# Performance work log

Hardware: AMD Instinct MI355X
Metric: run time of the kernel (lower is better)

## Reference

```python
import jax, jax.numpy as jnp
import numpy as np

B, NU, NI, D, L = 8, 1024, 2048, 64, 2
NUM_USERS, NUM_ITEMS = 100000, 50000


def setup_inputs() -> dict:
    key = jax.random.key(0)
    ks = jax.random.split(key, 9)
    return {
        "user_indices": jax.random.randint(ks[0], (B, NU), 0, NUM_USERS),
        "item_indices": jax.random.randint(ks[1], (B, NI), 0, NUM_ITEMS),
        "adj_matrices": jax.random.uniform(ks[2], (B, NU + NI, NU + NI), dtype=jnp.float32),
        "user_table": jax.random.normal(ks[3], (NUM_USERS, D), dtype=jnp.float32),
        "item_table": jax.random.normal(ks[4], (NUM_ITEMS, D), dtype=jnp.float32),
        "gc_w": jax.random.normal(ks[5], (L, D, D), dtype=jnp.float32) * 0.05,
        "gc_b": jax.random.normal(ks[6], (L, D), dtype=jnp.float32) * 0.05,
        "bi_w": jax.random.normal(ks[7], (L, D, D), dtype=jnp.float32) * 0.05,
        "bi_b": jax.random.normal(ks[8], (L, D), dtype=jnp.float32) * 0.05,
    }


def reference(user_indices, item_indices, adj_matrices, user_table, item_table, gc_w, gc_b, bi_w, bi_b):
    n_layers = gc_w.shape[0]

    def per_sample(u_idx, i_idx, adj):
        u_emb = user_table[u_idx]            # [NU, D]
        i_emb = item_table[i_idx]            # [NI, D]
        ego = jnp.concatenate([u_emb, i_emb], axis=0)  # [N, D]
        all_embs = [ego]
        for l in range(n_layers):
            side = adj @ ego                                        # [N, D]
            s = jax.nn.leaky_relu(side @ gc_w[l].T + gc_b[l])       # Linear(out,in) -> x @ W.T + b
            bi = jax.nn.leaky_relu((ego * side) @ bi_w[l].T + bi_b[l])
            ego = s + bi
            all_embs.append(ego)
        all_e = jnp.concatenate(all_embs, axis=1)                   # [N, D*(L+1)]
        u_g, i_g = all_e[: u_emb.shape[0]], all_e[u_emb.shape[0]:]
        scores = u_g @ i_g.T                                        # [NU, NI]
        return jax.nn.log_softmax(scores, axis=1)

    return jax.vmap(per_sample)(user_indices, item_indices, adj_matrices)
```

## Files before the change

kernel.cpp:

```cpp
#include <hip/hip_runtime.h>
#include <cstddef>

#define BB   8
#define NUU  1024
#define NII  2048
#define NTOT 3072
#define DD   64
#define KCAT 192

typedef __attribute__((ext_vector_type(8))) short bf16x8;
typedef __attribute__((ext_vector_type(4))) float f32x4;

__device__ __forceinline__ unsigned short f2bf(float f) {
  unsigned u = __float_as_uint(f);
  return (unsigned short)((u + 0x7fffu + ((u >> 16) & 1u)) >> 16);
}
__device__ __forceinline__ float bf2f(unsigned short s) {
  return __uint_as_float(((unsigned)s) << 16);
}
__device__ __forceinline__ uint4 pack8(float4 a, float4 b) {
  uint4 r;
  r.x = (unsigned)f2bf(a.x) | ((unsigned)f2bf(a.y) << 16);
  r.y = (unsigned)f2bf(a.z) | ((unsigned)f2bf(a.w) << 16);
  r.z = (unsigned)f2bf(b.x) | ((unsigned)f2bf(b.y) << 16);
  r.w = (unsigned)f2bf(b.z) | ((unsigned)f2bf(b.w) << 16);
  return r;
}
__device__ __forceinline__ bf16x8 u4_to_bf(uint4 u) {
  union { uint4 a; bf16x8 b; } x; x.a = u; return x.b;
}

__global__ __launch_bounds__(256) void transpose_w(
    const float* __restrict__ gcw, const float* __restrict__ biw,
    float* __restrict__ wT) {
  int g = blockIdx.x * 256 + threadIdx.x;
  int m = g >> 12, r = g & 4095;
  int k = r >> 6, d = r & 63;
  const float* src = (m < 2) ? gcw + m * 4096 : biw + (m - 2) * 4096;
  wT[g] = src[d * 64 + k];
}

__global__ __launch_bounds__(256) void gather_bf16(
    const int* __restrict__ uidx, const int* __restrict__ iidx,
    const float* __restrict__ utab, const float* __restrict__ itab,
    unsigned short* __restrict__ ecat) {
  int g = blockIdx.x * 256 + threadIdx.x;
  int node_g = g >> 2;
  int f0 = (g & 3) * 16;
  int b = node_g / NTOT;
  int row = node_g - b * NTOT;
  const float* src = (row < NUU) ? utab + (size_t)uidx[b * NUU + row] * DD
                                 : itab + (size_t)iidx[b * NII + row - NUU] * DD;
  const float4* s4 = reinterpret_cast<const float4*>(src + f0);
  uint4 lo = pack8(s4[0], s4[1]);
  uint4 hi = pack8(s4[2], s4[3]);
  uint4* dst = reinterpret_cast<uint4*>(ecat + (size_t)node_g * KCAT + f0);
  dst[0] = lo; dst[1] = hi;
}

__global__ __launch_bounds__(256) void conv_t(
    const unsigned short* __restrict__ ecat, int c0,
    unsigned short* __restrict__ Et) {
  __shared__ unsigned short T[64][65];
  const int tid = threadIdx.x;
  const int b = blockIdx.y;
  const int r0 = blockIdx.x * 64;
  {
    int nl = tid >> 2, fg = (tid & 3) * 16;
    const uint4* src = reinterpret_cast<const uint4*>(
        ecat + ((size_t)b * NTOT + r0 + nl) * KCAT + c0 + fg);
    uint4 v0 = src[0], v1 = src[1];
    unsigned short tmp[16];
    *reinterpret_cast<uint4*>(tmp) = v0;
    *reinterpret_cast<uint4*>(tmp + 8) = v1;
#pragma unroll
    for (int j = 0; j < 16; j++) T[fg + j][nl] = tmp[j];
  }
  __syncthreads();
  {
    int f = tid >> 2, ng = (tid & 3) * 16;
    unsigned short tmp[16];
#pragma unroll
    for (int j = 0; j < 16; j++) tmp[j] = T[f][ng + j];
    uint4* dst = reinterpret_cast<uint4*>(
        Et + ((size_t)b * DD + f) * NTOT + r0 + ng);
    dst[0] = *reinterpret_cast<uint4*>(tmp);
    dst[1] = *reinterpret_cast<uint4*>(tmp + 8);
  }
}

template <int CONV>
__global__ __launch_bounds__(256) void side_mfma_t(
    const float* __restrict__ adj, unsigned short* __restrict__ adjb,
    const unsigned short* __restrict__ Et, float* __restrict__ sp) {
  __shared__ __align__(16) unsigned short Bs[2][64][68];
  const int tid = threadIdx.x;
  const int w = tid >> 6, l = tid & 63;
  const int lane15 = l & 15, quad = l >> 4;
  const int b = blockIdx.z, kz = blockIdx.y;
  const int m0 = blockIdx.x * 128 + w * 16;
  const int kbase = kz * 768;
  const size_t row0 = (size_t)b * NTOT * NTOT +
                      (size_t)(m0 + lane15) * NTOT + kbase + quad * 8;
  const size_t row1 = row0 + (size_t)64 * NTOT;
  const float* A32_0 = adj + row0;
  const float* A32_1 = adj + row1;
  const unsigned short* A16_0 = adjb + row0;
  const unsigned short* A16_1 = adjb + row1;
  unsigned short* Aw_0 = adjb + row0;
  unsigned short* Aw_1 = adjb + row1;

  const int sf = tid >> 3, ss = (tid & 7) * 8;
  const unsigned short* Eb = Et + (size_t)b * DD * NTOT + kbase;
  uint4 p0 = *reinterpret_cast<const uint4*>(Eb + (size_t)sf * NTOT + ss);
  uint4 p1 = *reinterpret_cast<const uint4*>(Eb + (size_t)(sf + 32) * NTOT + ss);

  bf16x8 a0_0, a1_0, a0_1, a1_1;
  float4 f0_0, f1_0, f2_0, f3_0, f0_1, f1_1, f2_1, f3_1;
  if (CONV) {
    f0_0 = *reinterpret_cast<const float4*>(A32_0 + 0);
    f1_0 = *reinterpret_cast<const float4*>(A32_0 + 4);
    f2_0 = *reinterpret_cast<const float4*>(A32_0 + 32);
    f3_0 = *reinterpret_cast<const float4*>(A32_0 + 36);
    f0_1 = *reinterpret_cast<const float4*>(A32_1 + 0);
    f1_1 = *reinterpret_cast<const float4*>(A32_1 + 4);
    f2_1 = *reinterpret_cast<const float4*>(A32_1 + 32);
    f3_1 = *reinterpret_cast<const float4*>(A32_1 + 36);
  } else {
    a0_0 = *reinterpret_cast<const bf16x8*>(A16_0);
    a1_0 = *reinterpret_cast<const bf16x8*>(A16_0 + 32);
    a0_1 = *reinterpret_cast<const bf16x8*>(A16_1);
    a1_1 = *reinterpret_cast<const bf16x8*>(A16_1 + 32);
  }

  f32x4 acc[2][4];
#pragma unroll
  for (int s = 0; s < 2; s++)
#pragma unroll
    for (int t = 0; t < 4; t++) acc[s][t] = (f32x4){0.f, 0.f, 0.f, 0.f};

  for (int c = 0; c < 12; c++) {
    const int buf = c & 1;
    __syncthreads();
    *reinterpret_cast<uint4*>(&Bs[buf][sf][ss]) = p0;
    *reinterpret_cast<uint4*>(&Bs[buf][sf + 32][ss]) = p1;
    __syncthreads();

    if (CONV) {
      uint4 u0 = pack8(f0_0, f1_0), u1 = pack8(f2_0, f3_0);
      *reinterpret_cast<uint4*>(Aw_0 + c * 64) = u0;
      *reinterpret_cast<uint4*>(Aw_0 + c * 64 + 32) = u1;
      a0_0 = u4_to_bf(u0);
      a1_0 = u4_to_bf(u1);
      uint4 u2 = pack8(f0_1, f1_1), u3 = pack8(f2_1, f3_1);
      *reinterpret_cast<uint4*>(Aw_1 + c * 64) = u2;
      *reinterpret_cast<uint4*>(Aw_1 + c * 64 + 32) = u3;
      a0_1 = u4_to_bf(u2);
      a1_1 = u4_to_bf(u3);
    }

    bf16x8 na0_0, na1_0, na0_1, na1_1;
    if (c + 1 < 12) {
      p0 = *reinterpret_cast<const uint4*>(Eb + (size_t)sf * NTOT + (c + 1) * 64 + ss);
      p1 = *reinterpret_cast<const uint4*>(Eb + (size_t)(sf + 32) * NTOT + (c + 1) * 64 + ss);
      if (CONV) {
        f0_0 = *reinterpret_cast<const float4*>(A32_0 + (c + 1) * 64);
        f1_0 = *reinterpret_cast<const float4*>(A32_0 + (c + 1) * 64 + 4);
        f2_0 = *reinterpret_cast<const float4*>(A32_0 + (c + 1) * 64 + 32);
        f3_0 = *reinterpret_cast<const float4*>(A32_0 + (c + 1) * 64 + 36);
        f0_1 = *reinterpret_cast<const float4*>(A32_1 + (c + 1) * 64);
        f1_1 = *reinterpret_cast<const float4*>(A32_1 + (c + 1) * 64 + 4);
        f2_1 = *reinterpret_cast<const float4*>(A32_1 + (c + 1) * 64 + 32);
        f3_1 = *reinterpret_cast<const float4*>(A32_1 + (c + 1) * 64 + 36);
      } else {
        na0_0 = *reinterpret_cast<const bf16x8*>(A16_0 + (c + 1) * 64);
        na1_0 = *reinterpret_cast<const bf16x8*>(A16_0 + (c + 1) * 64 + 32);
        na0_1 = *reinterpret_cast<const bf16x8*>(A16_1 + (c + 1) * 64);
        na1_1 = *reinterpret_cast<const bf16x8*>(A16_1 + (c + 1) * 64 + 32);
      }
    }

#pragma unroll
    for (int t = 0; t < 4; t++) {
      bf16x8 b0 = *reinterpret_cast<const bf16x8*>(&Bs[buf][t * 16 + lane15][quad * 8]);
      acc[0][t] = __builtin_amdgcn_mfma_f32_16x16x32_bf16(a0_0, b0, acc[0][t], 0, 0, 0);
      acc[1][t] = __builtin_amdgcn_mfma_f32_16x16x32_bf16(a0_1, b0, acc[1][t], 0, 0, 0);
    }
#pragma unroll
    for (int t = 0; t < 4; t++) {
      bf16x8 b1 = *reinterpret_cast<const bf16x8*>(&Bs[buf][t * 16 + lane15][32 + quad * 8]);
      acc[0][t] = __builtin_amdgcn_mfma_f32_16x16x32_bf16(a1_0, b1, acc[0][t], 0, 0, 0);
      acc[1][t] = __builtin_amdgcn_mfma_f32_16x16x32_bf16(a1_1, b1, acc[1][t], 0, 0, 0);
    }
    if (!CONV && (c + 1 < 12)) {
      a0_0 = na0_0; a1_0 = na1_0; a0_1 = na0_1; a1_1 = na1_1;
    }
  }

  float* S = sp + ((size_t)kz * BB + b) * ((size_t)NTOT * DD);
#pragma unroll
  for (int s = 0; s < 2; s++)
#pragma unroll
    for (int t = 0; t < 4; t++)
#pragma unroll
      for (int r = 0; r < 4; r++)
        S[(size_t)(m0 + s * 64 + quad * 4 + r) * DD + t * 16 + lane15] =
            acc[s][t][r];
}

__global__ __launch_bounds__(256) void layer_post(
    const float* __restrict__ sp, unsigned short* __restrict__ ecat, int cin,
    const float* __restrict__ wTg, const float* __restrict__ wTb,
    const float* __restrict__ gcb, const float* __restrict__ bib) {
  __shared__ float wG[4096];
  __shared__ float wB[4096];
  __shared__ float rowS[4][64];
  __shared__ float rowE[4][64];
  const int tid = threadIdx.x;
#pragma unroll
  for (int i = 0; i < 16; i++) {
    int idx = tid + i * 256;
    wG[idx] = wTg[idx];
    wB[idx] = wTb[idx];
  }
  const int wv = tid >> 6, lane = tid & 63;
  const size_t row = (size_t)blockIdx.x * 4 + wv;
  const size_t off = row * DD + lane;
  const size_t P = (size_t)BB * NTOT * DD;
  float sv = sp[off] + sp[P + off] + sp[2 * P + off] + sp[3 * P + off];
  float ev = bf2f(ecat[row * KCAT + cin + lane]);
  rowS[wv][lane] = sv;
  rowE[wv][lane] = ev;
  __syncthreads();
  float sacc = gcb[lane];
  float bacc = bib[lane];
#pragma unroll 8
  for (int k = 0; k < 64; k++) {
    float sk = rowS[wv][k];
    float ek = rowE[wv][k];
    sacc += sk * wG[k * 64 + lane];
    bacc += (ek * sk) * wB[k * 64 + lane];
  }
  float s  = sacc > 0.f ? sacc : 0.01f * sacc;
  float bi = bacc > 0.f ? bacc : 0.01f * bacc;
  ecat[row * KCAT + cin + 64 + lane] = f2bf(s + bi);
}

__global__ __launch_bounds__(256) void scores_mfma(
    const unsigned short* __restrict__ ecat, float* __restrict__ out) {
  __shared__ __align__(16) unsigned short Ut[64 * KCAT];
  __shared__ __align__(16) unsigned short It[64 * KCAT];
  const int tid = threadIdx.x;
  const int w = tid >> 6, l = tid & 63;
  const int lane15 = l & 15, quad = l >> 4;
  const int b = blockIdx.z;
  const int u0 = blockIdx.y * 64;
  const int i0 = blockIdx.x * 64;
#pragma unroll
  for (int it = 0; it < 6; it++) {
    int idx = tid + it * 256;
    int row = idx / 24, c = idx - row * 24;
    int cs = c ^ (row & 7);
    uint4 vu = reinterpret_cast<const uint4*>(
        ecat + ((size_t)b * NTOT + u0 + row) * KCAT)[c];
    uint4 vi = reinterpret_cast<const uint4*>(
        ecat + ((size_t)b * NTOT + NUU + i0 + row) * KCAT)[c];
    reinterpret_cast<uint4*>(Ut)[row * 24 + cs] = vu;
    reinterpret_cast<uint4*>(It)[row * 24 + cs] = vi;
  }
  __syncthreads();
  f32x4 acc[4];
#pragma unroll
  for (int t = 0; t < 4; t++) acc[t] = (f32x4){0.f, 0.f, 0.f, 0.f};
  const int urow = w * 16 + lane15;
#pragma unroll
  for (int ks = 0; ks < 6; ks++) {
    int cu = (ks * 4 + quad) ^ (urow & 7);
    bf16x8 af = reinterpret_cast<const bf16x8*>(Ut)[urow * 24 + cu];
#pragma unroll
    for (int t = 0; t < 4; t++) {
      int irow = t * 16 + lane15;
      int ci = (ks * 4 + quad) ^ (irow & 7);
      bf16x8 bf = reinterpret_cast<const bf16x8*>(It)[irow * 24 + ci];
      acc[t] = __builtin_amdgcn_mfma_f32_16x16x32_bf16(af, bf, acc[t], 0, 0, 0);
    }
  }
  float* O = out + (size_t)b * NUU * NII;
#pragma unroll
  for (int t = 0; t < 4; t++)
#pragma unroll
    for (int r = 0; r < 4; r++)
      O[(size_t)(u0 + w * 16 + quad * 4 + r) * NII + i0 + t * 16 + lane15] =
          acc[t][r];
}

__global__ __launch_bounds__(256) void logsoftmax_kernel(float* __restrict__ out) {
  __shared__ float rm[4];
  __shared__ float rs[4];
  const int tid = threadIdx.x;
  const int lane = tid & 63, wv = tid >> 6;
  float* row = out + (size_t)blockIdx.x * NII;
  float4 v0 = *reinterpret_cast<const float4*>(row + tid * 4);
  float4 v1 = *reinterpret_cast<const float4*>(row + 1024 + tid * 4);
  float m = fmaxf(fmaxf(fmaxf(v0.x, v0.y), fmaxf(v0.z, v0.w)),
                  fmaxf(fmaxf(v1.x, v1.y), fmaxf(v1.z, v1.w)));
#pragma unroll
  for (int off = 32; off > 0; off >>= 1) m = fmaxf(m, __shfl_xor(m, off));
  if (lane == 0) rm[wv] = m;
  __syncthreads();
  m = fmaxf(fmaxf(rm[0], rm[1]), fmaxf(rm[2], rm[3]));
  float s = expf(v0.x - m) + expf(v0.y - m) + expf(v0.z - m) + expf(v0.w - m) +
            expf(v1.x - m) + expf(v1.y - m) + expf(v1.z - m) + expf(v1.w - m);
#pragma unroll
  for (int off = 32; off > 0; off >>= 1) s += __shfl_xor(s, off);
  if (lane == 0) rs[wv] = s;
  __syncthreads();
  float lse = m + logf(rs[0] + rs[1] + rs[2] + rs[3]);
  v0.x -= lse; v0.y -= lse; v0.z -= lse; v0.w -= lse;
  v1.x -= lse; v1.y -= lse; v1.z -= lse; v1.w -= lse;
  *reinterpret_cast<float4*>(row + tid * 4) = v0;
  *reinterpret_cast<float4*>(row + 1024 + tid * 4) = v1;
}

extern "C" void kernel_launch(void* const* d_in, const int* in_sizes, int n_in,
                              void* d_out, int out_size, void* d_ws, size_t ws_size,
                              hipStream_t stream) {
  (void)in_sizes; (void)n_in; (void)out_size; (void)ws_size;
  const int*   uidx = (const int*)d_in[0];
  const int*   iidx = (const int*)d_in[1];
  const float* adj  = (const float*)d_in[2];
  const float* utab = (const float*)d_in[3];
  const float* itab = (const float*)d_in[4];
  const float* gcw  = (const float*)d_in[5];
  const float* gcb  = (const float*)d_in[6];
  const float* biw  = (const float*)d_in[7];
  const float* bib  = (const float*)d_in[8];
  float* out = (float*)d_out;

  unsigned short* ecat = (unsigned short*)d_ws;
  unsigned short* Et   = ecat + (size_t)BB * NTOT * KCAT;
  unsigned short* adjb = Et + (size_t)BB * DD * NTOT;
  float* sp = (float*)d_out;
  const size_t P = (size_t)BB * NTOT * DD;
  float* wT = (float*)d_out + 4 * P;

  transpose_w<<<dim3(64), 256, 0, stream>>>(gcw, biw, wT);
  gather_bf16<<<dim3(BB * NTOT * 4 / 256), 256, 0, stream>>>(uidx, iidx, utab, itab, ecat);
  conv_t<<<dim3(48, BB), 256, 0, stream>>>(ecat, 0, Et);
  side_mfma_t<1><<<dim3(24, 4, BB), 256, 0, stream>>>(adj, adjb, Et, sp);
  layer_post<<<dim3(BB * NTOT / 4), 256, 0, stream>>>(sp, ecat, 0, wT, wT + 2 * 4096, gcb, bib);
  conv_t<<<dim3(48, BB), 256, 0, stream>>>(ecat, 64, Et);
  side_mfma_t<0><<<dim3(24, 4, BB), 256, 0, stream>>>(adj, adjb, Et, sp);
  layer_post<<<dim3(BB * NTOT / 4), 256, 0, stream>>>(sp, ecat, 64, wT + 4096, wT + 3 * 4096, gcb + 64, bib + 64);
  scores_mfma<<<dim3(32, 16, BB), 256, 0, stream>>>(ecat, out);
  logsoftmax_kernel<<<dim3(BB * NUU), 256, 0, stream>>>(out);
}
```

Before: 625.7 us.

## Fuse scores with log-softmax in LDS and fuse gather with transpose

Score computation and log-softmax are merged: each block computes 16 user rows against all items via MFMA, stages the scores in a large LDS buffer, and writes normalized output once, removing the extra read and rewrite of the big output. The gather, first-layer transpose and weight transpose are combined into one kernel to cut launches and a global round trip. The large LDS allocation limits occupancy to about one block per CU, and item embeddings are re-read by every block.

Result: slower. 651.8 us (+4.2%).

```diff
diff --git a/kernel.cpp b/kernel.cpp
--- a/kernel.cpp
+++ b/kernel.cpp
@@ -30,32 +30,52 @@
   union { uint4 a; bf16x8 b; } x; x.a = u; return x.b;
 }
 
-__global__ __launch_bounds__(256) void transpose_w(
-    const float* __restrict__ gcw, const float* __restrict__ biw,
-    float* __restrict__ wT) {
-  int g = blockIdx.x * 256 + threadIdx.x;
-  int m = g >> 12, r = g & 4095;
-  int k = r >> 6, d = r & 63;
-  const float* src = (m < 2) ? gcw + m * 4096 : biw + (m - 2) * 4096;
-  wT[g] = src[d * 64 + k];
-}
-
-__global__ __launch_bounds__(256) void gather_bf16(
+__global__ __launch_bounds__(256) void gather_t(
     const int* __restrict__ uidx, const int* __restrict__ iidx,
     const float* __restrict__ utab, const float* __restrict__ itab,
-    unsigned short* __restrict__ ecat) {
-  int g = blockIdx.x * 256 + threadIdx.x;
-  int node_g = g >> 2;
-  int f0 = (g & 3) * 16;
-  int b = node_g / NTOT;
-  int row = node_g - b * NTOT;
-  const float* src = (row < NUU) ? utab + (size_t)uidx[b * NUU + row] * DD
-                                 : itab + (size_t)iidx[b * NII + row - NUU] * DD;
-  const float4* s4 = reinterpret_cast<const float4*>(src + f0);
-  uint4 lo = pack8(s4[0], s4[1]);
-  uint4 hi = pack8(s4[2], s4[3]);
-  uint4* dst = reinterpret_cast<uint4*>(ecat + (size_t)node_g * KCAT + f0);
-  dst[0] = lo; dst[1] = hi;
+    const float* __restrict__ gcw, const float* __restrict__ biw,
+    unsigned short* __restrict__ ecat, unsigned short* __restrict__ Et,
+    float* __restrict__ wT) {
+  const int tid = threadIdx.x;
+  if (blockIdx.x >= 384) {
+    for (int i = tid; i < 16384; i += 256) {
+      int m = i >> 12, r = i & 4095;
+      int k = r >> 6, d = r & 63;
+      const float* src = (m < 2) ? gcw + m * 4096 : biw + (m - 2) * 4096;
+      wT[i] = src[d * 64 + k];
+    }
+    return;
+  }
+  __shared__ unsigned short T[64][65];
+  const int b = blockIdx.x / 48;
+  const int r0 = (blockIdx.x % 48) * 64;
+  {
+    int nl = tid >> 2, f0 = (tid & 3) * 16;
+    int row = r0 + nl;
+    const float* src = (row < NUU) ? utab + (size_t)uidx[b * NUU + row] * DD
+                                   : itab + (size_t)iidx[b * NII + row - NUU] * DD;
+    const float4* s4 = reinterpret_cast<const float4*>(src + f0);
+    uint4 lo = pack8(s4[0], s4[1]);
+    uint4 hi = pack8(s4[2], s4[3]);
+    uint4* dst = reinterpret_cast<uint4*>(ecat + ((size_t)b * NTOT + row) * KCAT + f0);
+    dst[0] = lo; dst[1] = hi;
+    unsigned short tmp[16];
+    *reinterpret_cast<uint4*>(tmp) = lo;
+    *reinterpret_cast<uint4*>(tmp + 8) = hi;
+#pragma unroll
+    for (int j = 0; j < 16; j++) T[f0 + j][nl] = tmp[j];
+  }
+  __syncthreads();
+  {
+    int f = tid >> 2, ng = (tid & 3) * 16;
+    unsigned short tmp[16];
+#pragma unroll
+    for (int j = 0; j < 16; j++) tmp[j] = T[f][ng + j];
+    uint4* dst = reinterpret_cast<uint4*>(
+        Et + ((size_t)b * DD + f) * NTOT + r0 + ng);
+    dst[0] = *reinterpret_cast<uint4*>(tmp);
+    dst[1] = *reinterpret_cast<uint4*>(tmp + 8);
+  }
 }
 
 __global__ __launch_bounds__(256) void conv_t(
@@ -246,80 +266,75 @@
   ecat[row * KCAT + cin + 64 + lane] = f2bf(s + bi);
 }
 
-__global__ __launch_bounds__(256) void scores_mfma(
+__global__ __launch_bounds__(256) void scores_lsm(
     const unsigned short* __restrict__ ecat, float* __restrict__ out) {
-  __shared__ __align__(16) unsigned short Ut[64 * KCAT];
-  __shared__ __align__(16) unsigned short It[64 * KCAT];
+  __shared__ float S[16][NII];
   const int tid = threadIdx.x;
   const int w = tid >> 6, l = tid & 63;
   const int lane15 = l & 15, quad = l >> 4;
-  const int b = blockIdx.z;
-  const int u0 = blockIdx.y * 64;
-  const int i0 = blockIdx.x * 64;
-#pragma unroll
-  for (int it = 0; it < 6; it++) {
-    int idx = tid + it * 256;
-    int row = idx / 24, c = idx - row * 24;
-    int cs = c ^ (row & 7);
-    uint4 vu = reinterpret_cast<const uint4*>(
-        ecat + ((size_t)b * NTOT + u0 + row) * KCAT)[c];
-    uint4 vi = reinterpret_cast<const uint4*>(
-        ecat + ((size_t)b * NTOT + NUU + i0 + row) * KCAT)[c];
-    reinterpret_cast<uint4*>(Ut)[row * 24 + cs] = vu;
-    reinterpret_cast<uint4*>(It)[row * 24 + cs] = vi;
+  const int b = blockIdx.y;
+  const int u0 = blockIdx.x * 16;
+
+  bf16x8 af[6];
+  const unsigned short* U =
+      ecat + ((size_t)b * NTOT + u0 + lane15) * KCAT + quad * 8;
+#pragma unroll
+  for (int ks = 0; ks < 6; ks++)
+    af[ks] = *reinterpret_cast<const bf16x8*>(U + ks * 32);
+
+  const unsigned short* I =
+      ecat + ((size_t)b * NTOT + NUU) * KCAT + quad * 8;
+  bf16x8 cur[6], nxt[6];
+  {
+    const unsigned short* Ir = I + (size_t)(w * 16 + lane15) * KCAT;
+#pragma unroll
+    for (int ks = 0; ks < 6; ks++)
+      cur[ks] = *reinterpret_cast<const bf16x8*>(Ir + ks * 32);
+  }
+  for (int ch = 0; ch < 32; ch++) {
+    if (ch + 1 < 32) {
+      const unsigned short* Ir =
+          I + (size_t)((ch + 1) * 64 + w * 16 + lane15) * KCAT;
+#pragma unroll
+      for (int ks = 0; ks < 6; ks++)
+        nxt[ks] = *reinterpret_cast<const bf16x8*>(Ir + ks * 32);
+    }
+    f32x4 acc = (f32x4){0.f, 0.f, 0.f, 0.f};
+#pragma unroll
+    for (int ks = 0; ks < 6; ks++)
+      acc = __builtin_amdgcn_mfma_f32_16x16x32_bf16(af[ks], cur[ks], acc, 0, 0, 0);
+    const int ic = ch * 64 + w * 16 + lane15;
+#pragma unroll
+    for (int r = 0; r < 4; r++) S[quad * 4 + r][ic] = acc[r];
+#pragma unroll
+    for (int ks = 0; ks < 6; ks++) cur[ks] = nxt[ks];
   }
   __syncthreads();
-  f32x4 acc[4];
-#pragma unroll
-  for (int t = 0; t < 4; t++) acc[t] = (f32x4){0.f, 0.f, 0.f, 0.f};
-  const int urow = w * 16 + lane15;
-#pragma unroll
-  for (int ks = 0; ks < 6; ks++) {
-    int cu = (ks * 4 + quad) ^ (urow & 7);
-    bf16x8 af = reinterpret_cast<const bf16x8*>(Ut)[urow * 24 + cu];
-#pragma unroll
-    for (int t = 0; t < 4; t++) {
-      int irow = t * 16 + lane15;
-      int ci = (ks * 4 + quad) ^ (irow & 7);
-      bf16x8 bf = reinterpret_cast<const bf16x8*>(It)[irow * 24 + ci];
-      acc[t] = __builtin_amdgcn_mfma_f32_16x16x32_bf16(af, bf, acc[t], 0, 0, 0);
-    }
-  }
-  float* O = out + (size_t)b * NUU * NII;
-#pragma unroll
-  for (int t = 0; t < 4; t++)
-#pragma unroll
-    for (int r = 0; r < 4; r++)
-      O[(size_t)(u0 + w * 16 + quad * 4 + r) * NII + i0 + t * 16 + lane15] =
-          acc[t][r];
-}
-
-__global__ __launch_bounds__(256) void logsoftmax_kernel(float* __restrict__ out) {
-  __shared__ float rm[4];
-  __shared__ float rs[4];
-  const int tid = threadIdx.x;
-  const int lane = tid & 63, wv = tid >> 6;
-  float* row = out + (size_t)blockIdx.x * NII;
-  float4 v0 = *reinterpret_cast<const float4*>(row + tid * 4);
-  float4 v1 = *reinterpret_cast<const float4*>(row + 1024 + tid * 4);
-  float m = fmaxf(fmaxf(fmaxf(v0.x, v0.y), fmaxf(v0.z, v0.w)),
-                  fmaxf(fmaxf(v1.x, v1.y), fmaxf(v1.z, v1.w)));
-#pragma unroll
-  for (int off = 32; off > 0; off >>= 1) m = fmaxf(m, __shfl_xor(m, off));
-  if (lane == 0) rm[wv] = m;
-  __syncthreads();
-  m = fmaxf(fmaxf(rm[0], rm[1]), fmaxf(rm[2], rm[3]));
-  float s = expf(v0.x - m) + expf(v0.y - m) + expf(v0.z - m) + expf(v0.w - m) +
-            expf(v1.x - m) + expf(v1.y - m) + expf(v1.z - m) + expf(v1.w - m);
-#pragma unroll
-  for (int off = 32; off > 0; off >>= 1) s += __shfl_xor(s, off);
-  if (lane == 0) rs[wv] = s;
-  __syncthreads();
-  float lse = m + logf(rs[0] + rs[1] + rs[2] + rs[3]);
-  v0.x -= lse; v0.y -= lse; v0.z -= lse; v0.w -= lse;
-  v1.x -= lse; v1.y -= lse; v1.z -= lse; v1.w -= lse;
-  *reinterpret_cast<float4*>(row + tid * 4) = v0;
-  *reinterpret_cast<float4*>(row + 1024 + tid * 4) = v1;
+  for (int rr = 0; rr < 4; rr++) {
+    const int row = w * 4 + rr;
+    float v[32];
+    float m = -3.4e38f;
+#pragma unroll
+    for (int j = 0; j < 32; j++) {
+      v[j] = S[row][j * 64 + l];
+      m = fmaxf(m, v[j]);
+    }
+#pragma unroll
+    for (int off = 32; off > 0; off >>= 1) m = fmaxf(m, __shfl_xor(m, off));
+    float s = 0.f;
+#pragma unroll
+    for (int j = 0; j < 32; j++) s += expf(v[j] - m);
+#pragma unroll
+    for (int off = 32; off > 0; off >>= 1) s += __shfl_xor(s, off);
+    const float lse = m + logf(s);
+    float* orow = out + ((size_t)b * NUU + u0 + row) * NII;
+#pragma unroll
+    for (int j = 0; j < 8; j++) {
+      float4 q = *reinterpret_cast<const float4*>(&S[row][j * 256 + l * 4]);
+      q.x -= lse; q.y -= lse; q.z -= lse; q.w -= lse;
+      *reinterpret_cast<float4*>(orow + j * 256 + l * 4) = q;
+    }
+  }
 }
 
 extern "C" void kernel_launch(void* const* d_in, const int* in_sizes, int n_in,
@@ -344,14 +359,11 @@
   const size_t P = (size_t)BB * NTOT * DD;
   float* wT = (float*)d_out + 4 * P;
 
-  transpose_w<<<dim3(64), 256, 0, stream>>>(gcw, biw, wT);
-  gather_bf16<<<dim3(BB * NTOT * 4 / 256), 256, 0, stream>>>(uidx, iidx, utab, itab, ecat);
-  conv_t<<<dim3(48, BB), 256, 0, stream>>>(ecat, 0, Et);
+  gather_t<<<dim3(385), 256, 0, stream>>>(uidx, iidx, utab, itab, gcw, biw, ecat, Et, wT);
   side_mfma_t<1><<<dim3(24, 4, BB), 256, 0, stream>>>(adj, adjb, Et, sp);
   layer_post<<<dim3(BB * NTOT / 4), 256, 0, stream>>>(sp, ecat, 0, wT, wT + 2 * 4096, gcb, bib);
   conv_t<<<dim3(48, BB), 256, 0, stream>>>(ecat, 64, Et);
   side_mfma_t<0><<<dim3(24, 4, BB), 256, 0, stream>>>(adj, adjb, Et, sp);
   layer_post<<<dim3(BB * NTOT / 4), 256, 0, stream>>>(sp, ecat, 64, wT + 4096, wT + 3 * 4096, gcb + 64, bib + 64);
-  scores_mfma<<<dim3(32, 16, BB), 256, 0, stream>>>(ecat, out);
-  logsoftmax_kernel<<<dim3(BB * NUU), 256, 0, stream>>>(out);
-}
+  scores_lsm<<<dim3(64, BB), 256, 0, stream>>>(ecat, out);
+}
```
